# Optimization experiments

Hardware: AMD Instinct MI355X
Metric: run time of the kernel (lower is better)

Reference implementation:

```python
import jax, jax.numpy as jnp
import numpy as np

B, S, C = 1, 6, 128
Hf, Wf = 56, 100            # feature map (stride-8 of 448x800)
IMG_H, IMG_W = 448, 800
Z, Y, X = 128, 8, 128
BOUNDS = (-50.0, 50.0, -5.0, 5.0, -50.0, 50.0)
CENTROID = (0.0, 0.1, 0.0)
EPS = 1e-6


def _voxel_centers():
    # ref-frame (cam0) coordinates of voxel centers, Vox_util.Mem2Ref of gridcloud3d
    xmin, xmax = BOUNDS[0] + CENTROID[0], BOUNDS[1] + CENTROID[0]
    ymin, ymax = BOUNDS[2] + CENTROID[1], BOUNDS[3] + CENTROID[1]
    zmin, zmax = BOUNDS[4] + CENTROID[2], BOUNDS[5] + CENTROID[2]
    vsx, vsy, vsz = (xmax - xmin) / X, (ymax - ymin) / Y, (zmax - zmin) / Z
    zi, yi, xi = jnp.meshgrid(jnp.arange(Z), jnp.arange(Y), jnp.arange(X), indexing='ij')
    xr = xmin + vsx * 0.5 + xi.astype(jnp.float32) * vsx
    yr = ymin + vsy * 0.5 + yi.astype(jnp.float32) * vsy
    zr = zmin + vsz * 0.5 + zi.astype(jnp.float32) * vsz
    return jnp.stack([xr.reshape(-1), yr.reshape(-1), zr.reshape(-1)], axis=-1)  # (N,3), N=Z*Y*X


def setup_inputs() -> dict:
    key = jax.random.key(0)
    k1, k2 = jax.random.split(key)
    cam_feat = jax.random.normal(k1, (B, S, C, Hf, Wf), dtype=jnp.float32)
    # intrinsics: fx=fy=500, principal point at image center
    K = np.zeros((B, S, 4, 4), np.float32)
    K[..., 0, 0] = 500.0; K[..., 1, 1] = 500.0
    K[..., 0, 2] = IMG_W / 2.0; K[..., 1, 2] = IMG_H / 2.0
    K[..., 2, 2] = 1.0; K[..., 3, 3] = 1.0
    # surround-view rig: rotate about y (camera-frame vertical) by 2*pi*s/S
    ang = np.arange(S) * (2.0 * np.pi / S)
    c, s = np.cos(ang).astype(np.float32), np.sin(ang).astype(np.float32)
    R = np.zeros((B, S, 3, 3), np.float32)
    R[..., 0, 0] = c; R[..., 0, 2] = s; R[..., 1, 1] = 1.0
    R[..., 2, 0] = -s; R[..., 2, 2] = c
    t = np.stack([0.5 * s, np.full(S, -1.0, np.float32), 0.5 * c], axis=-1)[None].astype(np.float32)
    conv_w = jax.random.normal(k2, (C, C * Y, 3, 3), dtype=jnp.float32) * 0.02
    return {
        'cam_feat': cam_feat,
        'intrins': jnp.asarray(K),
        'rots': jnp.asarray(R),
        'trans': jnp.asarray(t),
        'conv_w': conv_w,
    }


def reference(cam_feat, intrins, rots, trans, conv_w):
    Bn, Sn = cam_feat.shape[:2]
    BS = Bn * Sn
    # velo_T_cams = [R|t]; cam0_T_camXs = inv(velo_T_cams[:,0]) @ velo_T_cams
    velo_T = (jnp.zeros((Bn, Sn, 4, 4), cam_feat.dtype)
              .at[..., :3, :3].set(rots)
              .at[..., :3, 3].set(trans)
              .at[..., 3, 3].set(1.0))
    cam0_T_camXs = jnp.einsum('bij,bsjk->bsik', jnp.linalg.inv(velo_T[:, 0]), velo_T)
    camXs_T_cam0 = jnp.linalg.inv(cam0_T_camXs)  # (B,S,4,4)
    # scale_intrinsics to feature resolution
    sx, sy = Wf / float(IMG_W), Hf / float(IMG_H)
    Kf = (jnp.zeros((Bn, Sn, 4, 4), cam_feat.dtype)
          .at[..., 0, 0].set(intrins[..., 0, 0] * sx)
          .at[..., 1, 1].set(intrins[..., 1, 1] * sy)
          .at[..., 0, 2].set(intrins[..., 0, 2] * sx)
          .at[..., 1, 2].set(intrins[..., 1, 2] * sy)
          .at[..., 2, 2].set(1.0).at[..., 3, 3].set(1.0))
    pixB_T_cam0 = jnp.einsum('bsij,bsjk->bsik', Kf, camXs_T_cam0).reshape(BS, 4, 4)
    camXs_T_cam0 = camXs_T_cam0.reshape(BS, 4, 4)

    xyz = _voxel_centers()                                   # (N,3)
    xyz1 = jnp.concatenate([xyz, jnp.ones((xyz.shape[0], 1), xyz.dtype)], axis=-1)  # (N,4)
    cam_pts = jnp.einsum('pij,nj->pni', camXs_T_cam0, xyz1)  # (BS,N,4)
    z = cam_pts[..., 2]
    pix = jnp.einsum('pij,nj->pni', pixB_T_cam0, xyz1)       # (BS,N,4)
    denom = jnp.maximum(pix[..., 2:3], EPS)
    x = pix[..., 0] / denom[..., 0]
    y = pix[..., 1] / denom[..., 0]
    valid = (x > -0.5) & (x < Wf - 0.5) & (y > -0.5) & (y < Hf - 0.5) & (z > 0.0)

    # normalize_grid2d + grid_sample(align_corners=False) unnormalization
    gx = jnp.clip(2.0 * x / (Wf - 1) - 1.0, -2.0, 2.0)
    gy = jnp.clip(2.0 * y / (Hf - 1) - 1.0, -2.0, 2.0)
    ux = ((gx + 1.0) * Wf - 1.0) * 0.5
    uy = ((gy + 1.0) * Hf - 1.0) * 0.5
    x0f, y0f = jnp.floor(ux), jnp.floor(uy)
    wx, wy = ux - x0f, uy - y0f
    x0i, y0i = x0f.astype(jnp.int32), y0f.astype(jnp.int32)

    feat = cam_feat.reshape(BS, C, Hf * Wf)

    def corner(xi, yi, w):
        inb = (xi >= 0) & (xi < Wf) & (yi >= 0) & (yi < Hf)  # zeros padding
        idx = jnp.clip(yi, 0, Hf - 1) * Wf + jnp.clip(xi, 0, Wf - 1)
        v = jnp.take_along_axis(feat, idx[:, None, :], axis=2)  # (BS,C,N)
        return v * (w * inb.astype(w.dtype))[:, None, :]

    vals = (corner(x0i, y0i, (1 - wx) * (1 - wy))
            + corner(x0i + 1, y0i, wx * (1 - wy))
            + corner(x0i, y0i + 1, (1 - wx) * wy)
            + corner(x0i + 1, y0i + 1, wx * wy))
    vals = vals * valid[:, None, :].astype(vals.dtype)
    feat_mems = vals.reshape(Bn, Sn, C, Z, Y, X)

    # reduce_masked_mean over cameras
    mask = (jnp.abs(feat_mems) > 0).astype(feat_mems.dtype)
    feat_mem = jnp.sum(feat_mems * mask, axis=1) / (EPS + jnp.sum(mask, axis=1))  # (B,C,Z,Y,X)

    # BEV compress: permute(0,1,3,2,4) -> (B, C*Y, Z, X), conv3x3 + InstanceNorm + GELU
    bev = jnp.transpose(feat_mem, (0, 1, 3, 2, 4)).reshape(Bn, C * Y, Z, X)
    out = jax.lax.conv_general_dilated(bev, conv_w, (1, 1), 'SAME',
                                       dimension_numbers=('NCHW', 'OIHW', 'NCHW'))
    mu = out.mean(axis=(2, 3), keepdims=True)
    var = out.var(axis=(2, 3), keepdims=True)
    out = (out - mu) * jax.lax.rsqrt(var + 1e-5)
    return jax.nn.gelu(out, approximate=False)
```

## Files before the change

### kernel.cpp

```cpp
#include <hip/hip_runtime.h>
#include <cmath>

#define SNUM 6
#define CNUM 128
#define HF 56
#define WF 100
#define HW (HF*WF)
#define ZN 128
#define YN 8
#define XN 128
#define NVOX (ZN*YN*XN)

typedef __attribute__((ext_vector_type(8))) short bf16x8;
typedef __attribute__((ext_vector_type(4))) float f32x4;
typedef __attribute__((ext_vector_type(4))) int   i32x4;

__device__ __forceinline__ unsigned short f2bf(float f) {
    unsigned u = __builtin_bit_cast(unsigned, f);
    unsigned r = (u + 0x7FFFu + ((u >> 16) & 1u)) >> 16;
    return (unsigned short)r;
}
__device__ __forceinline__ float bf2f(unsigned short h) {
    unsigned u = (unsigned)h << 16;
    return __builtin_bit_cast(float, u);
}

__global__ void k_setup(const float* __restrict__ intrins,
                        const float* __restrict__ rots,
                        const float* __restrict__ trans,
                        float* __restrict__ mats) {
    int s = threadIdx.x;
    if (s >= SNUM) return;
    float R0[9], Rs[9], t0[3], ts[3];
    for (int i = 0; i < 9; ++i) { R0[i] = rots[i]; Rs[i] = rots[s*9 + i]; }
    for (int i = 0; i < 3; ++i) { t0[i] = trans[i]; ts[i] = trans[s*3 + i]; }
    float M[3][4];
    float d0 = t0[0]-ts[0], d1 = t0[1]-ts[1], d2 = t0[2]-ts[2];
    for (int i = 0; i < 3; ++i) {
        for (int j = 0; j < 3; ++j)
            M[i][j] = Rs[0*3+i]*R0[0*3+j] + Rs[1*3+i]*R0[1*3+j] + Rs[2*3+i]*R0[2*3+j];
        M[i][3] = Rs[0*3+i]*d0 + Rs[1*3+i]*d1 + Rs[2*3+i]*d2;
    }
    const float sx = (float)WF/800.0f, sy = (float)HF/448.0f;
    float fx = intrins[s*16 + 0]*sx, fy = intrins[s*16 + 5]*sy;
    float cx = intrins[s*16 + 2]*sx, cy = intrins[s*16 + 6]*sy;
    float* o = mats + s*24;
    for (int j = 0; j < 4; ++j) {
        o[0*4+j]      = M[0][j];
        o[1*4+j]      = M[1][j];
        o[2*4+j]      = M[2][j];
        o[12 + 0*4+j] = fx*M[0][j] + cx*M[2][j];
        o[12 + 1*4+j] = fy*M[1][j] + cy*M[2][j];
        o[12 + 2*4+j] = M[2][j];
    }
}

__global__ __launch_bounds__(256) void k_tfeat(const float* __restrict__ cf,
                                               unsigned short* __restrict__ featT) {
    __shared__ float t[32][33];
    int s = blockIdx.z;
    int p0 = blockIdx.x * 32, c0 = blockIdx.y * 32;
    int tx = threadIdx.x, ty = threadIdx.y;
#pragma unroll
    for (int k = 0; k < 4; ++k) {
        int r = ty + k*8;
        t[r][tx] = cf[((size_t)s*CNUM + c0 + r)*HW + p0 + tx];
    }
    __syncthreads();
#pragma unroll
    for (int k = 0; k < 4; ++k) {
        int r = ty + k*8;
        featT[((size_t)s*HW + p0 + r)*CNUM + c0 + tx] = f2bf(t[tx][r]);
    }
}

__global__ __launch_bounds__(256) void k_geo(const float* __restrict__ mats,
                                             float* __restrict__ uv) {
#pragma clang fp contract(off)
    int n = blockIdx.x * 256 + threadIdx.x;
    int zi = n >> 10, yi = (n >> 7) & 7, xi = n & 127;
    float xr = -49.609375f + (float)xi * 0.78125f;
    float yr = (-4.9f + 0.625f) + (float)yi * 1.25f;
    float zr = -49.609375f + (float)zi * 0.78125f;
#pragma unroll
    for (int s = 0; s < SNUM; ++s) {
        const float* m = mats + s*24;
        float zc = m[8]*xr  + m[9]*yr  + m[10]*zr + m[11];
        float ph = m[12]*xr + m[13]*yr + m[14]*zr + m[15];
        float qh = m[16]*xr + m[17]*yr + m[18]*zr + m[19];
        float denom = fmaxf(zc, 1e-6f);
        float px = ph / denom, py = qh / denom;
        bool valid = (px > -0.5f) & (px < (float)WF - 0.5f) &
                     (py > -0.5f) & (py < (float)HF - 0.5f) & (zc > 0.0f);
        float ux = -10000.0f, uy = -10000.0f;
        if (valid) {
            float gx = 2.0f*px/((float)WF - 1.0f) - 1.0f;
            float gy = 2.0f*py/((float)HF - 1.0f) - 1.0f;
            gx = fminf(fmaxf(gx, -2.0f), 2.0f);
            gy = fminf(fmaxf(gy, -2.0f), 2.0f);
            ux = ((gx + 1.0f)*(float)WF - 1.0f)*0.5f;
            uy = ((gy + 1.0f)*(float)HF - 1.0f)*0.5f;
        }
        uv[(n*SNUM + s)*2]     = ux;
        uv[(n*SNUM + s)*2 + 1] = uy;
    }
}

__global__ __launch_bounds__(256) void k_sample(const unsigned short* __restrict__ featT,
                                                const float* __restrict__ uv,
                                                unsigned short* __restrict__ bevin) {
#pragma clang fp contract(off)
    __shared__ float xch[16][132];
    const int tid = threadIdx.x;
    const int b = blockIdx.x;
    const int z = b >> 6, x0 = (b & 63) * 2;
    const int cl = tid & 15, vs = tid >> 4;
    const int y = vs >> 1, xs = vs & 1;
    const int n = z*1024 + y*128 + x0 + xs;
    const bf16x8 zz8 = {0,0,0,0,0,0,0,0};
    float sum[8], cnt[8];
#pragma unroll
    for (int k = 0; k < 8; ++k) { sum[k] = 0.0f; cnt[k] = 0.0f; }
    for (int s = 0; s < SNUM; ++s) {
        float2 u = ((const float2*)uv)[n*SNUM + s];
        if (u.x < -999.0f) continue;
        float x0f = floorf(u.x), y0f = floorf(u.y);
        float wx = u.x - x0f, wy = u.y - y0f;
        int ix = (int)x0f, iy = (int)y0f;
        float w00 = (1.0f-wx)*(1.0f-wy), w10 = wx*(1.0f-wy);
        float w01 = (1.0f-wx)*wy,        w11 = wx*wy;
        bool bx0 = (ix >= 0) & (ix < WF);
        bool bx1 = (ix >= -1) & (ix < WF-1);
        bool by0 = (iy >= 0) & (iy < HF);
        bool by1 = (iy >= -1) & (iy < HF-1);
        bool c00 = bx0 & by0, c10 = bx1 & by0, c01 = bx0 & by1, c11 = bx1 & by1;
        const unsigned short* fb = featT + (size_t)s * (HW*CNUM) + cl*8;
        long r0 = (long)(iy*WF + ix) * CNUM;
        bf16x8 v00 = c00 ? *(const bf16x8*)(fb + r0)                 : zz8;
        bf16x8 v10 = c10 ? *(const bf16x8*)(fb + r0 + CNUM)          : zz8;
        bf16x8 v01 = c01 ? *(const bf16x8*)(fb + r0 + WF*CNUM)       : zz8;
        bf16x8 v11 = c11 ? *(const bf16x8*)(fb + r0 + WF*CNUM + CNUM): zz8;
#pragma unroll
        for (int k = 0; k < 8; ++k) {
            float v = 0.0f;
            v = v + w00 * bf2f((unsigned short)v00[k]);
            v = v + w10 * bf2f((unsigned short)v10[k]);
            v = v + w01 * bf2f((unsigned short)v01[k]);
            v = v + w11 * bf2f((unsigned short)v11[k]);
            sum[k] += v;
            cnt[k] += (v != 0.0f) ? 1.0f : 0.0f;
        }
    }
#pragma unroll
    for (int k = 0; k < 8; ++k)
        xch[vs][cl*8 + k] = sum[k] / (1e-6f + cnt[k]);
    __syncthreads();
#pragma unroll
    for (int j = 0; j < 4; ++j) {
        int m = tid + j*256;
        int xs2 = m >> 9;
        int r = m & 511;
        int c = (2*r) >> 3, y0 = (2*r) & 7;
        float v0 = xch[y0*2 + xs2][c];
        float v1 = xch[(y0+1)*2 + xs2][c];
        unsigned pk = (unsigned)f2bf(v0) | ((unsigned)f2bf(v1) << 16);
        ((unsigned*)bevin)[(size_t)(z*128 + x0 + xs2)*512 + r] = pk;
    }
}

__global__ __launch_bounds__(256) void k_wprep(const float* __restrict__ w,
                                               unsigned short* __restrict__ w2) {
    int i = blockIdx.x*256 + threadIdx.x;
    if (i >= 9*128*1024) return;
    int ci = i & 1023; int rest = i >> 10; int co = rest & 127; int tap = rest >> 7;
    w2[i] = f2bf(w[((size_t)co*1024 + ci)*9 + tap]);
}

__global__ __launch_bounds__(128, 1) void k_conv_mfma(
        const unsigned short* __restrict__ bevin,
        const unsigned short* __restrict__ w2,
        float* __restrict__ out) {
    __shared__ unsigned short lds[2][12*66*8];
    const int tid  = threadIdx.x;
    const int z0   = blockIdx.x;
    const int coh  = blockIdx.y >> 1;
    const int xh   = blockIdx.y & 1;
    const int lane = tid & 63, wr = tid >> 6;
    const int co_base = coh*64 + wr*32;
    const int l15 = lane & 15, lhi = lane >> 4;

    if (tid < 24) {
        int bf = tid & 1, row = tid >> 1;
        *(i32x4*)&lds[bf][(row*66 + (xh ? 65 : 0))*8] = i32x4{0,0,0,0};
    }

    f32x4 acc[2][4];
#pragma unroll
    for (int f = 0; f < 2; ++f)
#pragma unroll
        for (int nf = 0; nf < 4; ++nf) acc[f][nf] = f32x4{0.f,0.f,0.f,0.f};

    const unsigned short* aw0 = w2 + ((size_t)(co_base      + l15))*1024 + lhi*8;
    const unsigned short* aw1 = w2 + ((size_t)(co_base + 16 + l15))*1024 + lhi*8;

    bf16x8 afr0[18], afr1[18];
    i32x4 pre[6], preh;
    bool  pv[6], phv;

    const int h_row  = tid >> 1;
    const int h_side = tid & 1;
    const int h_zz   = z0 - 1 + (h_row >> 2);
    const int h_kg   = h_row & 3;
    const int h_x    = xh*64 - 1 + h_side*65;
    const bool h_ok  = (tid < 24) && ((unsigned)h_zz < 128u) && ((unsigned)h_x < 128u);
    const int h_xpad = h_side ? 65 : 0;

#define A_LOAD(DST, CI0)                                                       \
    {                                                                          \
        _Pragma("unroll")                                                      \
        for (int t = 0; t < 9; ++t) {                                          \
            DST[t*2]   = *(const bf16x8*)(aw0 + (size_t)t*131072 + (CI0));     \
            DST[t*2+1] = *(const bf16x8*)(aw1 + (size_t)t*131072 + (CI0));     \
        }                                                                      \
    }
#define B_LOAD(CI0)                                                            \
    {                                                                          \
        _Pragma("unroll")                                                      \
        for (int j = 0; j < 6; ++j) {                                          \
            int i  = tid + j*128;                                              \
            int kg = i & 3, x = (i >> 2) & 63, zr = i >> 8;                    \
            int zz = z0 - 1 + zr;                                              \
            pv[j] = ((unsigned)zz < 128u);                                     \
            if (pv[j])                                                         \
                pre[j] = *(const i32x4*)&bevin[((size_t)(zz*128 + xh*64 + x))*1024 + (CI0) + kg*8]; \
        }                                                                      \
        phv = h_ok;                                                            \
        if (phv)                                                               \
            preh = *(const i32x4*)&bevin[((size_t)(h_zz*128 + h_x))*1024 + (CI0) + h_kg*8]; \
    }
#define B_WRITE(BUF)                                                           \
    {                                                                          \
        _Pragma("unroll")                                                      \
        for (int j = 0; j < 6; ++j) {                                          \
            int i  = tid + j*128;                                              \
            int kg = i & 3, x = (i >> 2) & 63, zr = i >> 8;                    \
            if (pv[j])                                                         \
                *(i32x4*)&lds[BUF][(((zr*4 + kg)*66) + 1 + x)*8] = pre[j];     \
        }                                                                      \
        if (phv)                                                               \
            *(i32x4*)&lds[BUF][((h_zz - (z0-1))*4*66 + h_kg*66 + h_xpad)*8] = preh; \
    }
#define COMPUTE(BUF, AFR)                                                      \
    {                                                                          \
        _Pragma("unroll")                                                      \
        for (int dz = 0; dz < 3; ++dz) {                                       \
            if ((unsigned)(z0 - 1 + dz) < 128u) {                              \
                _Pragma("unroll")                                              \
                for (int dx = 0; dx < 3; ++dx) {                               \
                    bf16x8 a0 = AFR[(dz*3+dx)*2];                              \
                    bf16x8 a1 = AFR[(dz*3+dx)*2+1];                            \
                    _Pragma("unroll")                                          \
                    for (int nf = 0; nf < 4; ++nf) {                           \
                        int xp = nf*16 + l15 + dx;                             \
                        bf16x8 bfr = *(const bf16x8*)&lds[BUF][(((dz*4 + lhi)*66) + xp)*8]; \
                        acc[0][nf] = __builtin_amdgcn_mfma_f32_16x16x32_bf16(a0, bfr, acc[0][nf], 0, 0, 0); \
                        acc[1][nf] = __builtin_amdgcn_mfma_f32_16x16x32_bf16(a1, bfr, acc[1][nf], 0, 0, 0); \
                    }                                                          \
                }                                                              \
            }                                                                  \
        }                                                                      \
    }

    B_LOAD(0);
    A_LOAD(afr0, 0);
    __syncthreads();
    B_WRITE(0);
    __syncthreads();

    for (int cc = 0; cc < 16; ++cc) {
        const int ci0 = cc*64;
        B_LOAD(ci0 + 32);
        A_LOAD(afr1, ci0 + 32);
        COMPUTE(0, afr0);
        B_WRITE(1);
        __syncthreads();
        if (cc < 15) {
            B_LOAD(ci0 + 64);
            A_LOAD(afr0, ci0 + 64);
        }
        COMPUTE(1, afr1);
        if (cc < 15) {
            B_WRITE(0);
            __syncthreads();
        }
    }

#pragma unroll
    for (int f = 0; f < 2; ++f)
#pragma unroll
        for (int nf = 0; nf < 4; ++nf)
#pragma unroll
            for (int r = 0; r < 4; ++r) {
                int co = co_base + f*16 + lhi*4 + r;
                out[(size_t)co*16384 + z0*128 + xh*64 + nf*16 + l15] = acc[f][nf][r];
            }
#undef A_LOAD
#undef B_LOAD
#undef B_WRITE
#undef COMPUTE
}

__global__ __launch_bounds__(256) void k_instnorm_stats(const float* __restrict__ out,
                                                        float* __restrict__ stats) {
    __shared__ float r1[256], r2[256];
    int co = blockIdx.x, tid = threadIdx.x;
    const float* p = out + (size_t)co*16384;
    float s1 = 0.0f, s2 = 0.0f;
    for (int i = tid; i < 16384; i += 256) { float v = p[i]; s1 += v; s2 += v*v; }
    r1[tid] = s1; r2[tid] = s2;
    __syncthreads();
    for (int off = 128; off > 0; off >>= 1) {
        if (tid < off) { r1[tid] += r1[tid+off]; r2[tid] += r2[tid+off]; }
        __syncthreads();
    }
    if (tid == 0) {
        float mean = r1[0] * (1.0f/16384.0f);
        float var  = r2[0] * (1.0f/16384.0f) - mean*mean;
        stats[co*2]   = mean;
        stats[co*2+1] = rsqrtf(var + 1e-5f);
    }
}

__global__ __launch_bounds__(256) void k_gelu(float* __restrict__ out,
                                              const float* __restrict__ stats) {
    int i = blockIdx.x*256 + threadIdx.x;
    int co = i >> 14;
    float v = out[i];
    float r = (v - stats[co*2]) * stats[co*2+1];
    out[i] = 0.5f * r * (1.0f + erff(r * 0.70710678118654752f));
}

extern "C" void kernel_launch(void* const* d_in, const int* in_sizes, int n_in,
                              void* d_out, int out_size, void* d_ws, size_t ws_size,
                              hipStream_t stream) {
    const float* cam_feat = (const float*)d_in[0];
    const float* intrins  = (const float*)d_in[1];
    const float* rots     = (const float*)d_in[2];
    const float* trans    = (const float*)d_in[3];
    const float* conv_w   = (const float*)d_in[4];
    float* out = (float*)d_out;
    float* ws  = (float*)d_ws;

    float* mats  = ws;
    float* uv    = ws + 160;
    unsigned short* featT = (unsigned short*)(uv + (size_t)NVOX*12);
    unsigned short* bevin = featT + (size_t)SNUM*HW*CNUM;
    unsigned short* w2    = bevin + (size_t)16384*1024;
    float* stats = (float*)(w2 + 9*128*1024);

    hipLaunchKernelGGL(k_setup, dim3(1), dim3(64), 0, stream, intrins, rots, trans, mats);
    hipLaunchKernelGGL(k_tfeat, dim3(HW/32, CNUM/32, SNUM), dim3(32,8), 0, stream, cam_feat, featT);
    hipLaunchKernelGGL(k_geo, dim3(NVOX/256), dim3(256), 0, stream, mats, uv);
    hipLaunchKernelGGL(k_wprep, dim3((9*128*1024 + 255)/256), dim3(256), 0, stream, conv_w, w2);
    hipLaunchKernelGGL(k_sample, dim3(8192), dim3(256), 0, stream, featT, uv, bevin);
    hipLaunchKernelGGL(k_conv_mfma, dim3(128, 4), dim3(128), 0, stream, bevin, w2, out);
    hipLaunchKernelGGL(k_instnorm_stats, dim3(128), dim3(256), 0, stream, out, stats);
    hipLaunchKernelGGL(k_gelu, dim3(8192), dim3(256), 0, stream, out, stats);
}
```

Measured before the change: 153.9 us.

## Split conv K-dimension across two wave pairs with LDS reduction

The MFMA conv block grows from 128 to 256 threads. The extra two waves each take half of the 1024 input channels (split-K), using separate LDS tiles, and their partial sums are combined through LDS before the store. This halves the serial K loop per wave and gives the CU more waves to hide latency with, at the cost of twice the LDS, an extra reduction step and more register pressure under launch_bounds(256,2). It also raises wave priority around the MFMA compute sections with s_setprio.

```diff
diff --git a/kernel.cpp b/kernel.cpp
--- a/kernel.cpp
+++ b/kernel.cpp
@@ -176,22 +176,25 @@
     w2[i] = f2bf(w[((size_t)co*1024 + ci)*9 + tap]);
 }
 
-__global__ __launch_bounds__(128, 1) void k_conv_mfma(
+__global__ __launch_bounds__(256, 2) void k_conv_mfma(
         const unsigned short* __restrict__ bevin,
         const unsigned short* __restrict__ w2,
         float* __restrict__ out) {
-    __shared__ unsigned short lds[2][12*66*8];
+    __shared__ unsigned short lds[2][2][12*66*8];
     const int tid  = threadIdx.x;
     const int z0   = blockIdx.x;
     const int coh  = blockIdx.y >> 1;
     const int xh   = blockIdx.y & 1;
-    const int lane = tid & 63, wr = tid >> 6;
+    const int lane = tid & 63, wid = tid >> 6;
+    const int wr = wid & 1, kh = wid >> 1;
     const int co_base = coh*64 + wr*32;
     const int l15 = lane & 15, lhi = lane >> 4;
 
-    if (tid < 24) {
-        int bf = tid & 1, row = tid >> 1;
-        *(i32x4*)&lds[bf][(row*66 + (xh ? 65 : 0))*8] = i32x4{0,0,0,0};
+    if (tid < 48) {
+        int khz = tid >= 24;
+        int t = tid - khz*24;
+        int bf = t & 1, row = t >> 1;
+        *(i32x4*)&lds[khz][bf][(row*66 + (xh ? 65 : 0))*8] = i32x4{0,0,0,0};
     }
 
     f32x4 acc[2][4];
@@ -200,19 +203,21 @@
 #pragma unroll
         for (int nf = 0; nf < 4; ++nf) acc[f][nf] = f32x4{0.f,0.f,0.f,0.f};
 
-    const unsigned short* aw0 = w2 + ((size_t)(co_base      + l15))*1024 + lhi*8;
-    const unsigned short* aw1 = w2 + ((size_t)(co_base + 16 + l15))*1024 + lhi*8;
+    const unsigned short* aw0 = w2 + ((size_t)(co_base      + l15))*1024 + kh*512 + lhi*8;
+    const unsigned short* aw1 = w2 + ((size_t)(co_base + 16 + l15))*1024 + kh*512 + lhi*8;
 
     bf16x8 afr0[18], afr1[18];
     i32x4 pre[6], preh;
     bool  pv[6], phv;
 
-    const int h_row  = tid >> 1;
-    const int h_side = tid & 1;
+    const int h_kh   = (tid >= 24) && (tid < 48);
+    const int h_t    = tid - (tid >= 24 ? 24 : 0);
+    const int h_row  = h_t >> 1;
+    const int h_side = h_t & 1;
     const int h_zz   = z0 - 1 + (h_row >> 2);
     const int h_kg   = h_row & 3;
     const int h_x    = xh*64 - 1 + h_side*65;
-    const bool h_ok  = (tid < 24) && ((unsigned)h_zz < 128u) && ((unsigned)h_x < 128u);
+    const bool h_ok  = (tid < 48) && ((unsigned)h_zz < 128u) && ((unsigned)h_x < 128u);
     const int h_xpad = h_side ? 65 : 0;
 
 #define A_LOAD(DST, CI0)                                                       \
@@ -227,31 +232,36 @@
     {                                                                          \
         _Pragma("unroll")                                                      \
         for (int j = 0; j < 6; ++j) {                                          \
-            int i  = tid + j*128;                                              \
-            int kg = i & 3, x = (i >> 2) & 63, zr = i >> 8;                    \
+            int i  = tid + j*256;                                              \
+            int ks = (i >= 768) ? 1 : 0;                                       \
+            int ii = i - ks*768;                                               \
+            int kg = ii & 3, x = (ii >> 2) & 63, zr = ii >> 8;                 \
             int zz = z0 - 1 + zr;                                              \
             pv[j] = ((unsigned)zz < 128u);                                     \
             if (pv[j])                                                         \
-                pre[j] = *(const i32x4*)&bevin[((size_t)(zz*128 + xh*64 + x))*1024 + (CI0) + kg*8]; \
+                pre[j] = *(const i32x4*)&bevin[((size_t)(zz*128 + xh*64 + x))*1024 + (CI0) + ks*512 + kg*8]; \
         }                                                                      \
         phv = h_ok;                                                            \
         if (phv)                                                               \
-            preh = *(const i32x4*)&bevin[((size_t)(h_zz*128 + h_x))*1024 + (CI0) + h_kg*8]; \
+            preh = *(const i32x4*)&bevin[((size_t)(h_zz*128 + h_x))*1024 + (CI0) + h_kh*512 + h_kg*8]; \
     }
 #define B_WRITE(BUF)                                                           \
     {                                                                          \
         _Pragma("unroll")                                                      \
         for (int j = 0; j < 6; ++j) {                                          \
-            int i  = tid + j*128;                                              \
-            int kg = i & 3, x = (i >> 2) & 63, zr = i >> 8;                    \
+            int i  = tid + j*256;                                              \
+            int ks = (i >= 768) ? 1 : 0;                                       \
+            int ii = i - ks*768;                                               \
+            int kg = ii & 3, x = (ii >> 2) & 63, zr = ii >> 8;                 \
             if (pv[j])                                                         \
-                *(i32x4*)&lds[BUF][(((zr*4 + kg)*66) + 1 + x)*8] = pre[j];     \
+                *(i32x4*)&lds[ks][BUF][(((zr*4 + kg)*66) + 1 + x)*8] = pre[j]; \
         }                                                                      \
         if (phv)                                                               \
-            *(i32x4*)&lds[BUF][((h_zz - (z0-1))*4*66 + h_kg*66 + h_xpad)*8] = preh; \
+            *(i32x4*)&lds[h_kh][BUF][(h_row*66 + h_xpad)*8] = preh;            \
     }
 #define COMPUTE(BUF, AFR)                                                      \
     {                                                                          \
+        __builtin_amdgcn_s_setprio(1);                                         \
         _Pragma("unroll")                                                      \
         for (int dz = 0; dz < 3; ++dz) {                                       \
             if ((unsigned)(z0 - 1 + dz) < 128u) {                              \
@@ -262,13 +272,14 @@
                     _Pragma("unroll")                                          \
                     for (int nf = 0; nf < 4; ++nf) {                           \
                         int xp = nf*16 + l15 + dx;                             \
-                        bf16x8 bfr = *(const bf16x8*)&lds[BUF][(((dz*4 + lhi)*66) + xp)*8]; \
+                        bf16x8 bfr = *(const bf16x8*)&lds[kh][BUF][(((dz*4 + lhi)*66) + xp)*8]; \
                         acc[0][nf] = __builtin_amdgcn_mfma_f32_16x16x32_bf16(a0, bfr, acc[0][nf], 0, 0, 0); \
                         acc[1][nf] = __builtin_amdgcn_mfma_f32_16x16x32_bf16(a1, bfr, acc[1][nf], 0, 0, 0); \
                     }                                                          \
                 }                                                              \
             }                                                                  \
         }                                                                      \
+        __builtin_amdgcn_s_setprio(0);                                         \
     }
 
     B_LOAD(0);
@@ -277,33 +288,48 @@
     B_WRITE(0);
     __syncthreads();
 
-    for (int cc = 0; cc < 16; ++cc) {
+    for (int cc = 0; cc < 8; ++cc) {
         const int ci0 = cc*64;
         B_LOAD(ci0 + 32);
         A_LOAD(afr1, ci0 + 32);
         COMPUTE(0, afr0);
         B_WRITE(1);
         __syncthreads();
-        if (cc < 15) {
+        if (cc < 7) {
             B_LOAD(ci0 + 64);
             A_LOAD(afr0, ci0 + 64);
         }
         COMPUTE(1, afr1);
-        if (cc < 15) {
+        if (cc < 7) {
             B_WRITE(0);
             __syncthreads();
         }
     }
 
-#pragma unroll
-    for (int f = 0; f < 2; ++f)
-#pragma unroll
-        for (int nf = 0; nf < 4; ++nf)
-#pragma unroll
-            for (int r = 0; r < 4; ++r) {
-                int co = co_base + f*16 + lhi*4 + r;
-                out[(size_t)co*16384 + z0*128 + xh*64 + nf*16 + l15] = acc[f][nf][r];
-            }
+    __syncthreads();
+    float* lds_f = (float*)&lds[0][0][0];
+    if (kh == 1) {
+#pragma unroll
+        for (int f = 0; f < 2; ++f)
+#pragma unroll
+            for (int nf = 0; nf < 4; ++nf)
+#pragma unroll
+                for (int r = 0; r < 4; ++r)
+                    lds_f[wr*2048 + (f*16 + lhi*4 + r)*64 + nf*16 + l15] = acc[f][nf][r];
+    }
+    __syncthreads();
+    if (kh == 0) {
+#pragma unroll
+        for (int f = 0; f < 2; ++f)
+#pragma unroll
+            for (int nf = 0; nf < 4; ++nf)
+#pragma unroll
+                for (int r = 0; r < 4; ++r) {
+                    int co = co_base + f*16 + lhi*4 + r;
+                    float v = acc[f][nf][r] + lds_f[wr*2048 + (f*16 + lhi*4 + r)*64 + nf*16 + l15];
+                    out[(size_t)co*16384 + z0*128 + xh*64 + nf*16 + l15] = v;
+                }
+    }
 #undef A_LOAD
 #undef B_LOAD
 #undef B_WRITE
@@ -363,7 +389,7 @@
     hipLaunchKernelGGL(k_geo, dim3(NVOX/256), dim3(256), 0, stream, mats, uv);
     hipLaunchKernelGGL(k_wprep, dim3((9*128*1024 + 255)/256), dim3(256), 0, stream, conv_w, w2);
     hipLaunchKernelGGL(k_sample, dim3(8192), dim3(256), 0, stream, featT, uv, bevin);
-    hipLaunchKernelGGL(k_conv_mfma, dim3(128, 4), dim3(128), 0, stream, bevin, w2, out);
+    hipLaunchKernelGGL(k_conv_mfma, dim3(128, 4), dim3(256), 0, stream, bevin, w2, out);
     hipLaunchKernelGGL(k_instnorm_stats, dim3(128), dim3(256), 0, stream, out, stats);
     hipLaunchKernelGGL(k_gelu, dim3(8192), dim3(256), 0, stream, out, stats);
 }
```

After: 174.5 us. +13.4%, slower.

## Pipeline conv weight loads per dz row and pad LDS rows against bank conflicts

Applied to the files above, without the earlier changes.

The MFMA conv kernel now keeps only two 6-fragment weight buffers in registers, one per dz row, instead of two 18-fragment buffers. It software-pipelines the global weight loads one dz step ahead of the compute. The LDS row stride is padded from 528 to 532 elements and split into 8-byte accesses, to reduce bank conflicts on the B-fragment reads. Compute sections are also wrapped in s_setprio. The intent is lower register pressure and fewer LDS conflicts, at the cost of shorter load-latency hiding for the weights and twice as many LDS instructions.

```diff
diff --git a/kernel.cpp b/kernel.cpp
--- a/kernel.cpp
+++ b/kernel.cpp
@@ -180,7 +180,7 @@
         const unsigned short* __restrict__ bevin,
         const unsigned short* __restrict__ w2,
         float* __restrict__ out) {
-    __shared__ unsigned short lds[2][12*66*8];
+    __shared__ __align__(16) unsigned short lds[2][12*532];
     const int tid  = threadIdx.x;
     const int z0   = blockIdx.x;
     const int coh  = blockIdx.y >> 1;
@@ -191,7 +191,9 @@
 
     if (tid < 24) {
         int bf = tid & 1, row = tid >> 1;
-        *(i32x4*)&lds[bf][(row*66 + (xh ? 65 : 0))*8] = i32x4{0,0,0,0};
+        int off = row*532 + (xh ? 65*8 : 0);
+        *(int2*)&lds[bf][off]     = int2{0,0};
+        *(int2*)&lds[bf][off + 4] = int2{0,0};
     }
 
     f32x4 acc[2][4];
@@ -203,7 +205,7 @@
     const unsigned short* aw0 = w2 + ((size_t)(co_base      + l15))*1024 + lhi*8;
     const unsigned short* aw1 = w2 + ((size_t)(co_base + 16 + l15))*1024 + lhi*8;
 
-    bf16x8 afr0[18], afr1[18];
+    bf16x8 aC[6], aN[6];
     i32x4 pre[6], preh;
     bool  pv[6], phv;
 
@@ -213,14 +215,14 @@
     const int h_kg   = h_row & 3;
     const int h_x    = xh*64 - 1 + h_side*65;
     const bool h_ok  = (tid < 24) && ((unsigned)h_zz < 128u) && ((unsigned)h_x < 128u);
-    const int h_xpad = h_side ? 65 : 0;
-
-#define A_LOAD(DST, CI0)                                                       \
+    const int h_off  = h_row*532 + (h_side ? 65*8 : 0);
+
+#define A3(DST, DZ, CI0)                                                       \
     {                                                                          \
         _Pragma("unroll")                                                      \
-        for (int t = 0; t < 9; ++t) {                                          \
-            DST[t*2]   = *(const bf16x8*)(aw0 + (size_t)t*131072 + (CI0));     \
-            DST[t*2+1] = *(const bf16x8*)(aw1 + (size_t)t*131072 + (CI0));     \
+        for (int t = 0; t < 3; ++t) {                                          \
+            DST[t*2]   = *(const bf16x8*)(aw0 + (size_t)((DZ)*3+t)*131072 + (CI0)); \
+            DST[t*2+1] = *(const bf16x8*)(aw1 + (size_t)((DZ)*3+t)*131072 + (CI0)); \
         }                                                                      \
     }
 #define B_LOAD(CI0)                                                            \
@@ -244,35 +246,41 @@
         for (int j = 0; j < 6; ++j) {                                          \
             int i  = tid + j*128;                                              \
             int kg = i & 3, x = (i >> 2) & 63, zr = i >> 8;                    \
-            if (pv[j])                                                         \
-                *(i32x4*)&lds[BUF][(((zr*4 + kg)*66) + 1 + x)*8] = pre[j];     \
-        }                                                                      \
-        if (phv)                                                               \
-            *(i32x4*)&lds[BUF][((h_zz - (z0-1))*4*66 + h_kg*66 + h_xpad)*8] = preh; \
-    }
-#define COMPUTE(BUF, AFR)                                                      \
+            if (pv[j]) {                                                       \
+                int off = (zr*4 + kg)*532 + (1 + x)*8;                         \
+                *(int2*)&lds[BUF][off]     = int2{pre[j][0], pre[j][1]};       \
+                *(int2*)&lds[BUF][off + 4] = int2{pre[j][2], pre[j][3]};       \
+            }                                                                  \
+        }                                                                      \
+        if (phv) {                                                             \
+            *(int2*)&lds[BUF][h_off]     = int2{preh[0], preh[1]};             \
+            *(int2*)&lds[BUF][h_off + 4] = int2{preh[2], preh[3]};             \
+        }                                                                      \
+    }
+#define CDZ(DZ, BUF, AFR)                                                      \
     {                                                                          \
-        _Pragma("unroll")                                                      \
-        for (int dz = 0; dz < 3; ++dz) {                                       \
-            if ((unsigned)(z0 - 1 + dz) < 128u) {                              \
+        if ((unsigned)(z0 - 1 + (DZ)) < 128u) {                                \
+            __builtin_amdgcn_s_setprio(1);                                     \
+            _Pragma("unroll")                                                  \
+            for (int dx = 0; dx < 3; ++dx) {                                   \
+                bf16x8 a0 = AFR[dx*2];                                         \
+                bf16x8 a1 = AFR[dx*2+1];                                       \
                 _Pragma("unroll")                                              \
-                for (int dx = 0; dx < 3; ++dx) {                               \
-                    bf16x8 a0 = AFR[(dz*3+dx)*2];                              \
-                    bf16x8 a1 = AFR[(dz*3+dx)*2+1];                            \
-                    _Pragma("unroll")                                          \
-                    for (int nf = 0; nf < 4; ++nf) {                           \
-                        int xp = nf*16 + l15 + dx;                             \
-                        bf16x8 bfr = *(const bf16x8*)&lds[BUF][(((dz*4 + lhi)*66) + xp)*8]; \
-                        acc[0][nf] = __builtin_amdgcn_mfma_f32_16x16x32_bf16(a0, bfr, acc[0][nf], 0, 0, 0); \
-                        acc[1][nf] = __builtin_amdgcn_mfma_f32_16x16x32_bf16(a1, bfr, acc[1][nf], 0, 0, 0); \
-                    }                                                          \
+                for (int nf = 0; nf < 4; ++nf) {                               \
+                    const unsigned short* bp = &lds[BUF][((DZ)*4 + lhi)*532 + (nf*16 + l15 + dx)*8]; \
+                    int2 blo = *(const int2*)bp;                               \
+                    int2 bhi = *(const int2*)(bp + 4);                         \
+                    bf16x8 bfr = __builtin_bit_cast(bf16x8, int4{blo.x, blo.y, bhi.x, bhi.y}); \
+                    acc[0][nf] = __builtin_amdgcn_mfma_f32_16x16x32_bf16(a0, bfr, acc[0][nf], 0, 0, 0); \
+                    acc[1][nf] = __builtin_amdgcn_mfma_f32_16x16x32_bf16(a1, bfr, acc[1][nf], 0, 0, 0); \
                 }                                                              \
             }                                                                  \
+            __builtin_amdgcn_s_setprio(0);                                     \
         }                                                                      \
     }
 
     B_LOAD(0);
-    A_LOAD(afr0, 0);
+    A3(aC, 0, 0);
     __syncthreads();
     B_WRITE(0);
     __syncthreads();
@@ -280,15 +288,16 @@
     for (int cc = 0; cc < 16; ++cc) {
         const int ci0 = cc*64;
         B_LOAD(ci0 + 32);
-        A_LOAD(afr1, ci0 + 32);
-        COMPUTE(0, afr0);
+        A3(aN, 1, ci0);      CDZ(0, 0, aC);
+        A3(aC, 2, ci0);      CDZ(1, 0, aN);
+        A3(aN, 0, ci0 + 32); CDZ(2, 0, aC);
         B_WRITE(1);
         __syncthreads();
-        if (cc < 15) {
-            B_LOAD(ci0 + 64);
-            A_LOAD(afr0, ci0 + 64);
-        }
-        COMPUTE(1, afr1);
+        if (cc < 15) B_LOAD(ci0 + 64);
+        A3(aC, 1, ci0 + 32); CDZ(0, 1, aN);
+        A3(aN, 2, ci0 + 32); CDZ(1, 1, aC);
+        if (cc < 15) A3(aC, 0, ci0 + 64);
+        CDZ(2, 1, aN);
         if (cc < 15) {
             B_WRITE(0);
             __syncthreads();
@@ -304,10 +313,10 @@
                 int co = co_base + f*16 + lhi*4 + r;
                 out[(size_t)co*16384 + z0*128 + xh*64 + nf*16 + l15] = acc[f][nf][r];
             }
-#undef A_LOAD
+#undef A3
 #undef B_LOAD
 #undef B_WRITE
-#undef COMPUTE
+#undef CDZ
 }
 
 __global__ __launch_bounds__(256) void k_instnorm_stats(const float* __restrict__ out,
```

Result: slower. 158.4 us (+3.0%).
